# Optimization experiments

Measured on AMD Instinct MI355X. Metric: run time of the kernel, lower is better.

The kernel has to match this reference:

```python
import jax, jax.numpy as jnp
import numpy as np
from jax import lax

# ---- config (mirrors cfg) ----
NUM_LEVELS = 4
DS = 2            # DS_FACTOR
T = 16            # TILE_SIZE
SR = 4            # SEARCH_RADIUS
PADD = 1
SW = 0.1          # SPATIAL_WEIGHT
GR = 2            # GAUSS_RADIUS
SIGMA = 1.0
SS = 2 * (SR + PADD) + 1      # 11: padded search grid
SSC = 2 * SR + 1              # 9: cropped search grid
WIN = T + 2 * (SR + PADD)     # 26: gathered window per tile

# ---- subpixel-refinement quadratic-fit filters (from __init__) ----
F_A11 = jnp.asarray(np.array([[1,-2,1],[2,-4,2],[1,-2,1]], np.float32) / 4.0)
F_A22 = jnp.asarray(np.array([[1,2,1],[-2,-4,-2],[1,2,1]], np.float32) / 4.0)
F_A12 = jnp.asarray(np.array([[1,0,-1],[0,0,0],[-1,0,1]], np.float32) / 4.0)
F_B1  = jnp.asarray(np.array([[-1,0,1],[-2,0,2],[-1,0,1]], np.float32) / 8.0)
F_B2  = jnp.asarray(np.array([[-1,-2,-1],[0,0,0],[1,2,1]], np.float32) / 8.0)
F_C   = jnp.asarray(np.array([[-1,2,-1],[2,12,2],[-1,2,-1]], np.float32) / 16.0)


def _gauss_kernel():
    ws = 2 * GR + 1
    ax = np.arange(ws, dtype=np.float32) - GR
    g = np.exp(-(ax ** 2) / (2.0 * SIGMA ** 2))
    k = np.outer(g, g)
    k = k / k.sum()
    return jnp.asarray(k, jnp.float32)


def _pyramid(x):
    """Gaussian pyramid: depthwise gaussian blur + avg-pool(ds) per level."""
    k = _gauss_kernel()[None, None]  # OIHW, C=1
    pad = (2 * GR + 1 - 1) // 2
    pyr = [x]
    for _ in range(NUM_LEVELS - 1):
        y = lax.conv_general_dilated(x, k, (1, 1), [(pad, pad), (pad, pad)],
                                     dimension_numbers=('NCHW', 'OIHW', 'NCHW'))
        n, c, h, w = y.shape
        x = y.reshape(n, c, h // DS, DS, w // DS, DS).mean(axis=(3, 5))
        pyr.append(x)
    return pyr


def _sdist_map():
    ax = (np.arange(SS, dtype=np.float32) - (SR + PADD)) / float(SS)
    return jnp.asarray(ax[:, None] ** 2 + ax[None, :] ** 2, jnp.float32)


def _step(init_offset, src, dst):
    """One pyramid-level block-matching step + subpixel refine."""
    n, nth, ntw, _ = init_offset.shape
    H, W = src.shape[2], src.shape[3]
    oy = jnp.round(init_offset[..., 0]).astype(jnp.int32)
    ox = jnp.round(init_offset[..., 1]).astype(jnp.int32)
    base_y = (jnp.arange(nth, dtype=jnp.int32) * T)[None, :, None]
    base_x = (jnp.arange(ntw, dtype=jnp.int32) * T)[None, None, :]
    y0 = base_y + oy - (SR + PADD)
    x0 = base_x + ox - (SR + PADD)
    Y = jnp.clip(y0[..., None] + jnp.arange(WIN), 0, H - 1)
    X = jnp.clip(x0[..., None] + jnp.arange(WIN), 0, W - 1)
    nidx = jnp.arange(n)[:, None, None, None, None]
    window = dst[:, 0][nidx, Y[..., :, None], X[..., None, :]]
    # source tiles [n,nth,ntw,T,T]
    src_t = src[:, 0].reshape(n, nth, T, ntw, T).transpose(0, 1, 3, 2, 4)
    # all SSxSS candidate tiles from the window (static slide indices)
    sl = jnp.arange(SS)[:, None] + jnp.arange(T)[None, :]  # [SS,T]
    cand = window[:, :, :, sl[:, None, :, None], sl[None, :, None, :]]  # [n,nth,ntw,SS,SS,T,T]
    adist = jnp.mean((cand - src_t[:, :, :, None, None]) ** 2, axis=(-2, -1))
    dist_full = adist + SW * _sdist_map()  # [n,nth,ntw,SS,SS]
    dist = dist_full[:, :, :, PADD:-PADD, PADD:-PADD].reshape(n, nth, ntw, SSC * SSC)
    min_dist = jnp.min(dist, axis=3)
    pk = jnp.argmin(dist, axis=3)
    py = pk // SSC
    px = pk % SSC
    offset = init_offset + jnp.stack([(py - SR).astype(jnp.float32),
                                      (px - SR).astype(jnp.float32)], axis=3)
    # RegionSelection: 3x3 neighborhood of dist_full around (py+PADD, px+PADD)
    ry = (py + PADD)[..., None] + jnp.arange(-1, 2)
    rx = (px + PADD)[..., None] + jnp.arange(-1, 2)
    tyi = jnp.arange(nth)[None, :, None, None, None]
    txi = jnp.arange(ntw)[None, None, :, None, None]
    yreg = dist_full[nidx, tyi, txi, ry[..., :, None], rx[..., None, :]]  # [n,nth,ntw,3,3]
    s = lambda f: jnp.sum(f * yreg, axis=(-2, -1))
    a11 = jax.nn.relu(s(F_A11))
    a22 = jax.nn.relu(s(F_A22))
    a12 = s(F_A12)
    b1 = s(F_B1)
    b2 = s(F_B2)
    det = a11 * a22 - a12 ** 2
    a12z = jnp.where(det < 0, jnp.zeros_like(a12), a12)
    mu_x = -(a22 * b1 - a12z * b2) / det
    mu_y = -(a11 * b2 - a12z * b1) / det
    mu_len = jnp.sqrt(mu_y ** 2 + mu_x ** 2)
    dx = jnp.where(mu_len < 1.0, mu_x, jnp.zeros_like(mu_x))
    dy = jnp.where(mu_len < 1.0, mu_y, jnp.zeros_like(mu_y))
    offset = offset.at[..., 0].add(dy).at[..., 1].add(dx)
    return offset, min_dist


def _inherit(prev_offset, nth, ntw, H, W):
    typ = jnp.arange(nth) // DS
    txp = jnp.arange(ntw) // DS
    off = DS * prev_offset[:, typ[:, None], txp[None, :], :]
    iy = (jnp.arange(nth, dtype=jnp.float32) * T)[None, :, None]
    ix = (jnp.arange(ntw, dtype=jnp.float32) * T)[None, None, :]
    dy = jnp.clip(off[..., 0] + iy, 0.0, float(H - T)) - iy
    dx = jnp.clip(off[..., 1] + ix, 0.0, float(W - T)) - ix
    return jnp.round(jnp.stack([dy, dx], axis=3))


def _align(src, dst):
    ps = _pyramid(src)
    pd = _pyramid(dst)
    offset = None
    min_dist = None
    for level in range(NUM_LEVELS - 1, -1, -1):
        s, d = ps[level], pd[level]
        n, _, h, w = s.shape
        nth = int(np.ceil(h / T))
        ntw = int(np.ceil(w / T))
        if level == NUM_LEVELS - 1:
            init = jnp.zeros((n, nth, ntw, 2), jnp.float32)
        else:
            init = _inherit(offset, nth, ntw, h, w)
        offset, min_dist = _step(init, s, d)
    # nearest-neighbor upsample by TILE_SIZE to per-pixel maps
    pixel_off = jnp.repeat(jnp.repeat(offset, T, axis=1), T, axis=2)   # [n,H,W,2]
    pixel_dist = jnp.repeat(jnp.repeat(min_dist, T, axis=1), T, axis=2)  # [n,H,W]
    return pixel_off, pixel_dist


def setup_inputs() -> dict:
    key = jax.random.key(0)
    k1, k2 = jax.random.split(key)
    src = jax.random.uniform(k1, (4, 1, 512, 512), jnp.float32)
    dst = jax.random.uniform(k2, (4, 1, 512, 512), jnp.float32)
    return {"src": src, "dst": dst}


def reference(src, dst):
    return _align(src, dst)
```

## Files before the change

### kernel.cpp

```cpp
#include <hip/hip_runtime.h>


#define NB 4
#define NPIX (NB * 512 * 512)

constexpr float H6[6] = {
    0.027244342f, 0.149345013f, 0.323410645f,
    0.323410645f, 0.149345013f, 0.027244342f
};

__global__ void __launch_bounds__(256, 4)
pyramid_kernel(const float* __restrict__ src, const float* __restrict__ dst,
               float* __restrict__ ws) {
    __shared__ float smem[8160];
    float* patch = smem;
    float* tmpH1 = smem + 5520;
    float* l1    = smem;
    float* tmpH2 = smem + 1232;
    float* l2    = smem + 1792;
    float* tmpH3 = smem + 2032;

    float* sL1 = ws;
    float* dL1 = sL1 + 4 * 65536;
    float* sL2 = dL1 + 4 * 65536;
    float* dL2 = sL2 + 4 * 16384;
    float* sL3 = dL2 + 4 * 16384;
    float* dL3 = sL3 + 4 * 4096;

    const int bx = blockIdx.x, by = blockIdx.y, z = blockIdx.z;
    const int t = threadIdx.x;
    const float* in = (z < 4) ? (src + (size_t)z * 262144) : (dst + (size_t)(z - 4) * 262144);
    float* oL1 = ((z < 4) ? sL1 : dL1) + (size_t)(z & 3) * 65536;
    float* oL2 = ((z < 4) ? sL2 : dL2) + (size_t)(z & 3) * 16384;
    float* oL3 = ((z < 4) ? sL3 : dL3) + (size_t)(z & 3) * 4096;

    {
        const int oy = by * 32 - 14, ox = bx * 64 - 14;
        for (int idx = t; idx < 5520; idx += 256) {
            int r = idx / 92, c = idx - r * 92;
            int gy = oy + r, gx = ox + c;
            float v = 0.f;
            if ((unsigned)gy < 512u && (unsigned)gx < 512u) v = in[gy * 512 + gx];
            patch[r * 92 + c] = v;
        }
    }
    __syncthreads();
    for (int idx = t; idx < 2640; idx += 256) {
        int r = idx / 44, v = idx - r * 44;
        const float* p = &patch[r * 92 + 2 * v];
        float a = 0.f;
        #pragma unroll
        for (int bq = 0; bq < 6; ++bq) a = fmaf(H6[bq], p[bq], a);
        tmpH1[r * 44 + v] = a;
    }
    __syncthreads();
    {
        const int oy = by * 16 - 6, ox = bx * 32 - 6;
        for (int idx = t; idx < 1232; idx += 256) {
            int u = idx / 44, v = idx - u * 44;
            float a = 0.f;
            int y1 = oy + u, x1 = ox + v;
            if ((unsigned)y1 < 256u && (unsigned)x1 < 256u) {
                #pragma unroll
                for (int bq = 0; bq < 6; ++bq) a = fmaf(H6[bq], tmpH1[(2 * u + bq) * 44 + v], a);
            }
            l1[u * 44 + v] = a;
        }
    }
    __syncthreads();
    {
        #pragma unroll
        for (int k = 0; k < 2; ++k) {
            int idx = t + k * 256;
            int u = idx >> 5, v = idx & 31;
            oL1[(by * 16 + u) * 256 + bx * 32 + v] = l1[(6 + u) * 44 + 6 + v];
        }
    }
    for (int idx = t; idx < 560; idx += 256) {
        int r = idx / 20, v = idx - r * 20;
        const float* p = &l1[r * 44 + 2 * v];
        float a = 0.f;
        #pragma unroll
        for (int bq = 0; bq < 6; ++bq) a = fmaf(H6[bq], p[bq], a);
        tmpH2[r * 20 + v] = a;
    }
    __syncthreads();
    {
        const int oy = by * 8 - 2, ox = bx * 16 - 2;
        if (t < 240) {
            int u = t / 20, v = t - u * 20;
            float a = 0.f;
            int y2 = oy + u, x2 = ox + v;
            if ((unsigned)y2 < 128u && (unsigned)x2 < 128u) {
                #pragma unroll
                for (int bq = 0; bq < 6; ++bq) a = fmaf(H6[bq], tmpH2[(2 * u + bq) * 20 + v], a);
            }
            l2[u * 20 + v] = a;
        }
    }
    __syncthreads();
    if (t < 128) {
        int u = t >> 4, v = t & 15;
        oL2[(by * 8 + u) * 128 + bx * 16 + v] = l2[(2 + u) * 20 + 2 + v];
    } else if (t < 224) {
        int idx = t - 128;
        int r = idx >> 3, v = idx & 7;
        const float* p = &l2[r * 20 + 2 * v];
        float a = 0.f;
        #pragma unroll
        for (int bq = 0; bq < 6; ++bq) a = fmaf(H6[bq], p[bq], a);
        tmpH3[r * 8 + v] = a;
    }
    __syncthreads();
    if (t < 32) {
        int u = t >> 3, v = t & 7;
        float a = 0.f;
        #pragma unroll
        for (int bq = 0; bq < 6; ++bq) a = fmaf(H6[bq], tmpH3[(2 * u + bq) * 8 + v], a);
        oL3[(by * 4 + u) * 64 + bx * 8 + v] = a;
    }
}

__device__ __forceinline__ void inherit_off(int ty, int tx, int H,
                                            float pary, float parx,
                                            float& dyf, float& dxf) {
    float iy = (float)(ty * 16), ix = (float)(tx * 16);
    dyf = rintf(fminf(fmaxf(2.f * pary + iy, 0.f), (float)(H - 16)) - iy);
    dxf = rintf(fminf(fmaxf(2.f * parx + ix, 0.f), (float)(H - 16)) - ix);
}

template<int NL>
__device__ __forceinline__ void load_win(const float* __restrict__ dimg, int H,
                                         int y0, int x0, float* win, int lt) {
    const int c = lt & 31;
    const int r0 = lt >> 5;
    constexpr int RSTEP = NL / 32;
    if (c < 26) {
        const int gx = min(max(x0 + c, 0), H - 1);
        #pragma unroll
        for (int k = 0; k < (26 + RSTEP - 1) / RSTEP; ++k) {
            const int rr = r0 + k * RSTEP;
            if (rr < 26) {
                const int gy = min(max(y0 + rr, 0), H - 1);
                win[rr * 28 + c] = dimg[gy * H + gx];
            }
        }
    }
}

template<bool FULL>
__device__ __forceinline__ void ssd_dist(const float* win, const float* st,
                                         float* dist, int lt) {
    const int dy = FULL ? (lt >> 4) : (lt >> 3);
    if (dy < 11) {
        float acc[11];
        #pragma unroll
        for (int q = 0; q < 11; ++q) acc[q] = 0.f;
        constexpr int ROWS = FULL ? 1 : 2;
        #pragma unroll
        for (int rr = 0; rr < ROWS; ++rr) {
            const int i = FULL ? (lt & 15) : ((lt & 7) * 2 + rr);
            float w[28], s[16];
            const float4* wp = (const float4*)&win[(dy + i) * 28];
            #pragma unroll
            for (int q = 0; q < 7; ++q) ((float4*)w)[q] = wp[q];
            const float4* sp = (const float4*)&st[i * 20];
            #pragma unroll
            for (int q = 0; q < 4; ++q) ((float4*)s)[q] = sp[q];
            #pragma unroll
            for (int dx = 0; dx < 11; ++dx) {
                #pragma unroll
                for (int j = 0; j < 16; ++j) {
                    float d = w[dx + j] - s[j];
                    acc[dx] = fmaf(d, d, acc[dx]);
                }
            }
        }
        constexpr int MMAX = FULL ? 8 : 4;
        #pragma unroll
        for (int m = 1; m <= MMAX; m <<= 1) {
            #pragma unroll
            for (int dx = 0; dx < 11; ++dx) acc[dx] += __shfl_xor(acc[dx], m);
        }
        const bool leader = FULL ? ((lt & 15) == 0) : ((lt & 7) == 0);
        if (leader) {
            float ay = (float)(dy - 5) * (1.f / 11.f);
            #pragma unroll
            for (int dx = 0; dx < 11; ++dx) {
                float ax = (float)(dx - 5) * (1.f / 11.f);
                dist[dy * 11 + dx] = acc[dx] * (1.f / 256.f) + 0.1f * (ay * ay + ax * ax);
            }
        }
    }
}

__device__ __forceinline__ void argmin_refine(const float* dist, int lt,
                                              float dyf, float dxf,
                                              float& roy, float& rox, float& rod) {
    const int l = lt & 63;
    float bv; int bk;
    {
        int k = l;
        int py = k / 9, px = k - (k / 9) * 9;
        bv = dist[(py + 1) * 11 + (px + 1)]; bk = k;
        k = l + 64;
        if (k < 81) {
            py = k / 9; px = k - (k / 9) * 9;
            float d = dist[(py + 1) * 11 + (px + 1)];
            if (d < bv) { bv = d; bk = k; }
        }
    }
    #pragma unroll
    for (int m = 1; m <= 32; m <<= 1) {
        float ov = __shfl_xor(bv, m);
        int   ok = __shfl_xor(bk, m);
        if (ov < bv || (ov == bv && ok < bk)) { bv = ov; bk = ok; }
    }
    {
        int py = bk / 9, px = bk - (bk / 9) * 9;
        float y00 = dist[(py + 0) * 11 + (px + 0)], y01 = dist[(py + 0) * 11 + (px + 1)], y02 = dist[(py + 0) * 11 + (px + 2)];
        float y10 = dist[(py + 1) * 11 + (px + 0)], y11 = dist[(py + 1) * 11 + (px + 1)], y12 = dist[(py + 1) * 11 + (px + 2)];
        float y20 = dist[(py + 2) * 11 + (px + 0)], y21 = dist[(py + 2) * 11 + (px + 1)], y22 = dist[(py + 2) * 11 + (px + 2)];

        float a11 = (y00 - 2.f * y01 + y02 + 2.f * y10 - 4.f * y11 + 2.f * y12 + y20 - 2.f * y21 + y22) * 0.25f;
        a11 = fmaxf(a11, 0.f);
        float a22 = (y00 + 2.f * y01 + y02 - 2.f * y10 - 4.f * y11 - 2.f * y12 + y20 + 2.f * y21 + y22) * 0.25f;
        a22 = fmaxf(a22, 0.f);
        float a12 = (y00 - y02 - y20 + y22) * 0.25f;
        float b1  = (-y00 + y02 - 2.f * y10 + 2.f * y12 - y20 + y22) * 0.125f;
        float b2  = (-y00 - 2.f * y01 - y02 + y20 + 2.f * y21 + y22) * 0.125f;

        float det  = a11 * a22 - a12 * a12;
        float a12z = (det < 0.f) ? 0.f : a12;
        float mu_x = -(a22 * b1 - a12z * b2) / det;
        float mu_y = -(a11 * b2 - a12z * b1) / det;
        float mu_len = sqrtf(mu_x * mu_x + mu_y * mu_y);
        float addx = (mu_len < 1.f) ? mu_x : 0.f;
        float addy = (mu_len < 1.f) ? mu_y : 0.f;

        roy = dyf + (float)(py - 4) + addy;
        rox = dxf + (float)(px - 4) + addx;
        rod = bv;
    }
}

__global__ void __launch_bounds__(256, 4)
step_chain_kernel(const float* __restrict__ src, const float* __restrict__ dst,
                  const float* __restrict__ ws, float* __restrict__ out) {
    __shared__ float smem[6520];

    const float* sL1 = ws;
    const float* dL1 = sL1 + 4 * 65536;
    const float* sL2 = dL1 + 4 * 65536;
    const float* dL2 = sL2 + 4 * 16384;
    const float* sL3 = dL2 + 4 * 16384;
    const float* dL3 = sL3 + 4 * 4096;

    const int gid = blockIdx.x;
    const int b   = gid >> 8;
    const int ty1 = (gid >> 4) & 15;
    const int tx1 = gid & 15;
    const int t    = threadIdx.x;
    const int slot = t >> 7;
    const int s_t  = t & 127;

    float* win_c  = smem;
    float* winA   = smem + 728 + (2 * slot + 0) * 728;
    float* winB   = smem + 728 + (2 * slot + 1) * 728;
    float* dist_c = smem + 3640;
    float* distA  = smem + 3768 + (2 * slot + 0) * 128;
    float* distB  = smem + 3768 + (2 * slot + 1) * 128;
    float* stL3 = smem + 4280;
    float* stL2 = smem + 4600;
    float* stL1 = smem + 4920;
    float* st0  = smem + 5240;

    const float* s0 = src + (size_t)b * 262144; const float* d0 = dst + (size_t)b * 262144;
    const float* s1 = sL1 + (size_t)b * 65536;  const float* d1 = dL1 + (size_t)b * 65536;
    const float* s2 = sL2 + (size_t)b * 16384;  const float* d2 = dL2 + (size_t)b * 16384;
    const float* s3 = sL3 + (size_t)b * 4096;   const float* d3 = dL3 + (size_t)b * 4096;

    {
        const int it = t & 63, r = it >> 2, q = t & 3;
        const int c = t >> 6;
        const int ty0 = 2 * ty1 + (c >> 1), tx0 = 2 * tx1 + (c & 1);
        const float4* p0 = (const float4*)(s0 + (size_t)(ty0 * 16 + r) * 512 + tx0 * 16);
        ((float4*)&st0[c * 320 + r * 20])[q] = p0[q];
        if (t < 64) {
            const float4* p = (const float4*)(s3 + (size_t)((ty1 >> 2) * 16 + r) * 64 + (tx1 >> 2) * 16);
            ((float4*)&stL3[r * 20])[q] = p[q];
        } else if (t < 128) {
            const float4* p = (const float4*)(s2 + (size_t)((ty1 >> 1) * 16 + r) * 128 + (tx1 >> 1) * 16);
            ((float4*)&stL2[r * 20])[q] = p[q];
        } else if (t < 192) {
            const float4* p = (const float4*)(s1 + (size_t)(ty1 * 16 + r) * 256 + tx1 * 16);
            ((float4*)&stL1[r * 20])[q] = p[q];
        }
    }

    float oy, ox, od;
    {
        load_win<256>(d3, 64, (ty1 >> 2) * 16 - 5, (tx1 >> 2) * 16 - 5, win_c, t);
        __syncthreads();
        ssd_dist<true>(win_c, stL3, dist_c, t);
        __syncthreads();
        argmin_refine(dist_c, t, 0.f, 0.f, oy, ox, od);
    }
    {
        float dyf, dxf; inherit_off(ty1 >> 1, tx1 >> 1, 128, oy, ox, dyf, dxf);
        load_win<256>(d2, 128, (ty1 >> 1) * 16 + (int)dyf - 5, (tx1 >> 1) * 16 + (int)dxf - 5, win_c, t);
        __syncthreads();
        ssd_dist<true>(win_c, stL2, dist_c, t);
        __syncthreads();
        argmin_refine(dist_c, t, dyf, dxf, oy, ox, od);
    }
    {
        float dyf, dxf; inherit_off(ty1, tx1, 256, oy, ox, dyf, dxf);
        load_win<256>(d1, 256, ty1 * 16 + (int)dyf - 5, tx1 * 16 + (int)dxf - 5, win_c, t);
        __syncthreads();
        ssd_dist<true>(win_c, stL1, dist_c, t);
        __syncthreads();
        argmin_refine(dist_c, t, dyf, dxf, oy, ox, od);
    }

    const int tyA = 2 * ty1,     txA = 2 * tx1 + slot;
    const int tyB = 2 * ty1 + 1, txB = 2 * tx1 + slot;
    float dyfA, dxfA, dyfB, dxfB;
    inherit_off(tyA, txA, 512, oy, ox, dyfA, dxfA);
    inherit_off(tyB, txB, 512, oy, ox, dyfB, dxfB);
    load_win<128>(d0, 512, tyA * 16 + (int)dyfA - 5, txA * 16 + (int)dxfA - 5, winA, s_t);
    load_win<128>(d0, 512, tyB * 16 + (int)dyfB - 5, txB * 16 + (int)dxfB - 5, winB, s_t);
    __syncthreads();
    ssd_dist<false>(winA, st0 + (0 * 2 + slot) * 320, distA, s_t);
    __syncthreads();
    ssd_dist<false>(winB, st0 + (1 * 2 + slot) * 320, distB, s_t);
    __syncthreads();

    const int r = s_t >> 3, c2 = (s_t & 7) * 2;
    {
        float oyA, oxA, odA;
        argmin_refine(distA, s_t, dyfA, dxfA, oyA, oxA, odA);
        int pyy = tyA * 16 + r, pxx = txA * 16 + c2;
        size_t pi = ((size_t)(b * 512 + pyy)) * 512 + pxx;
        float2 o; o.x = oyA; o.y = oxA;
        ((float2*)out)[pi]     = o;
        ((float2*)out)[pi + 1] = o;
        float2 dd; dd.x = odA; dd.y = odA;
        *(float2*)(out + (size_t)NPIX * 2 + pi) = dd;
    }
    {
        float oyB, oxB, odB;
        argmin_refine(distB, s_t, dyfB, dxfB, oyB, oxB, odB);
        int pyy = tyB * 16 + r, pxx = txB * 16 + c2;
        size_t pi = ((size_t)(b * 512 + pyy)) * 512 + pxx;
        float2 o; o.x = oyB; o.y = oxB;
        ((float2*)out)[pi]     = o;
        ((float2*)out)[pi + 1] = o;
        float2 dd; dd.x = odB; dd.y = odB;
        *(float2*)(out + (size_t)NPIX * 2 + pi) = dd;
    }
}

extern "C" void kernel_launch(void* const* d_in, const int* in_sizes, int n_in,
                              void* d_out, int out_size, void* d_ws, size_t ws_size,
                              hipStream_t stream) {
    const float* src = (const float*)d_in[0];
    const float* dst = (const float*)d_in[1];
    float* out = (float*)d_out;
    float* ws  = (float*)d_ws;

    hipLaunchKernelGGL(pyramid_kernel, dim3(8, 16, 8), dim3(256), 0, stream, src, dst, ws);
    hipLaunchKernelGGL(step_chain_kernel, dim3(1024), dim3(256), 0, stream, src, dst, ws, out);
}
```

Measured before the change: 104.5 us.

## Split coarse pyramid levels into a separate seed kernel to avoid redundant work

The coarse levels 3 and 2 of the block-matching chain used to be recomputed by every step_chain block, even though four blocks share the same level-2 tile and sixteen share the same level-3 tile. A new seed_kernel computes them once per level-2 tile and writes the offsets to workspace. step_chain_kernel then reads the seed offset and runs only levels 1 and 0. This removes duplicated coarse-level work and some shared memory, at the cost of an extra kernel launch and a global round trip.

```diff
diff --git a/kernel.cpp b/kernel.cpp
--- a/kernel.cpp
+++ b/kernel.cpp
@@ -3,6 +3,7 @@
 
 #define NB 4
 #define NPIX (NB * 512 * 512)
+#define OFFS_BASE 1212416
 
 constexpr float H6[6] = {
     0.027244342f, 0.149345013f, 0.323410645f,
@@ -245,16 +246,67 @@
 }
 
 __global__ void __launch_bounds__(256, 4)
-step_chain_kernel(const float* __restrict__ src, const float* __restrict__ dst,
-                  const float* __restrict__ ws, float* __restrict__ out) {
-    __shared__ float smem[6520];
-
-    const float* sL1 = ws;
-    const float* dL1 = sL1 + 4 * 65536;
-    const float* sL2 = dL1 + 4 * 65536;
+seed_kernel(const float* __restrict__ ws_ro, float* __restrict__ ws) {
+    __shared__ float smem[1496];
+    float* win_c  = smem;
+    float* dist_c = smem + 728;
+    float* stL3   = smem + 856;
+    float* stL2   = smem + 1176;
+
+    const float* sL2 = ws_ro + 4 * 65536 + 4 * 65536;
     const float* dL2 = sL2 + 4 * 16384;
     const float* sL3 = dL2 + 4 * 16384;
     const float* dL3 = sL3 + 4 * 4096;
+    float* offs = ws + OFFS_BASE;
+
+    const int gid = blockIdx.x;
+    const int b   = gid >> 6;
+    const int ty2 = (gid >> 3) & 7;
+    const int tx2 = gid & 7;
+    const int t   = threadIdx.x;
+
+    const float* s2 = sL2 + (size_t)b * 16384;  const float* d2 = dL2 + (size_t)b * 16384;
+    const float* s3 = sL3 + (size_t)b * 4096;   const float* d3 = dL3 + (size_t)b * 4096;
+
+    {
+        const int it = t & 63, r = it >> 2, q = t & 3;
+        if (t < 64) {
+            const float4* p = (const float4*)(s3 + (size_t)((ty2 >> 1) * 16 + r) * 64 + (tx2 >> 1) * 16);
+            ((float4*)&stL3[r * 20])[q] = p[q];
+        } else if (t < 128) {
+            const float4* p = (const float4*)(s2 + (size_t)(ty2 * 16 + r) * 128 + tx2 * 16);
+            ((float4*)&stL2[r * 20])[q] = p[q];
+        }
+    }
+
+    float oy, ox, od;
+    load_win<256>(d3, 64, (ty2 >> 1) * 16 - 5, (tx2 >> 1) * 16 - 5, win_c, t);
+    __syncthreads();
+    ssd_dist<true>(win_c, stL3, dist_c, t);
+    __syncthreads();
+    argmin_refine(dist_c, t, 0.f, 0.f, oy, ox, od);
+    {
+        float dyf, dxf; inherit_off(ty2, tx2, 128, oy, ox, dyf, dxf);
+        load_win<256>(d2, 128, ty2 * 16 + (int)dyf - 5, tx2 * 16 + (int)dxf - 5, win_c, t);
+        __syncthreads();
+        ssd_dist<true>(win_c, stL2, dist_c, t);
+        __syncthreads();
+        argmin_refine(dist_c, t, dyf, dxf, oy, ox, od);
+    }
+    if (t == 0) {
+        const int oi = ((b * 8 + ty2) * 8 + tx2) * 2;
+        offs[oi]     = oy;
+        offs[oi + 1] = ox;
+    }
+}
+
+__global__ void __launch_bounds__(256, 4)
+step_chain_kernel(const float* __restrict__ src, const float* __restrict__ dst,
+                  const float* __restrict__ ws, float* __restrict__ out) {
+    __shared__ float smem[5880];
+
+    const float* sL1 = ws;
+    const float* offs = ws + OFFS_BASE;
 
     const int gid = blockIdx.x;
     const int b   = gid >> 8;
@@ -270,15 +322,15 @@
     float* dist_c = smem + 3640;
     float* distA  = smem + 3768 + (2 * slot + 0) * 128;
     float* distB  = smem + 3768 + (2 * slot + 1) * 128;
-    float* stL3 = smem + 4280;
-    float* stL2 = smem + 4600;
-    float* stL1 = smem + 4920;
-    float* st0  = smem + 5240;
+    float* stL1 = smem + 4280;
+    float* st0  = smem + 4600;
 
     const float* s0 = src + (size_t)b * 262144; const float* d0 = dst + (size_t)b * 262144;
-    const float* s1 = sL1 + (size_t)b * 65536;  const float* d1 = dL1 + (size_t)b * 65536;
-    const float* s2 = sL2 + (size_t)b * 16384;  const float* d2 = dL2 + (size_t)b * 16384;
-    const float* s3 = sL3 + (size_t)b * 4096;   const float* d3 = dL3 + (size_t)b * 4096;
+    const float* s1 = sL1 + (size_t)b * 65536;
+    const float* d1 = sL1 + 4 * 65536 + (size_t)b * 65536;
+
+    const int oi = ((b * 8 + (ty1 >> 1)) * 8 + (tx1 >> 1)) * 2;
+    const float poy = offs[oi], pox = offs[oi + 1];
 
     {
         const int it = t & 63, r = it >> 2, q = t & 3;
@@ -287,12 +339,6 @@
         const float4* p0 = (const float4*)(s0 + (size_t)(ty0 * 16 + r) * 512 + tx0 * 16);
         ((float4*)&st0[c * 320 + r * 20])[q] = p0[q];
         if (t < 64) {
-            const float4* p = (const float4*)(s3 + (size_t)((ty1 >> 2) * 16 + r) * 64 + (tx1 >> 2) * 16);
-            ((float4*)&stL3[r * 20])[q] = p[q];
-        } else if (t < 128) {
-            const float4* p = (const float4*)(s2 + (size_t)((ty1 >> 1) * 16 + r) * 128 + (tx1 >> 1) * 16);
-            ((float4*)&stL2[r * 20])[q] = p[q];
-        } else if (t < 192) {
             const float4* p = (const float4*)(s1 + (size_t)(ty1 * 16 + r) * 256 + tx1 * 16);
             ((float4*)&stL1[r * 20])[q] = p[q];
         }
@@ -300,22 +346,7 @@
 
     float oy, ox, od;
     {
-        load_win<256>(d3, 64, (ty1 >> 2) * 16 - 5, (tx1 >> 2) * 16 - 5, win_c, t);
-        __syncthreads();
-        ssd_dist<true>(win_c, stL3, dist_c, t);
-        __syncthreads();
-        argmin_refine(dist_c, t, 0.f, 0.f, oy, ox, od);
-    }
-    {
-        float dyf, dxf; inherit_off(ty1 >> 1, tx1 >> 1, 128, oy, ox, dyf, dxf);
-        load_win<256>(d2, 128, (ty1 >> 1) * 16 + (int)dyf - 5, (tx1 >> 1) * 16 + (int)dxf - 5, win_c, t);
-        __syncthreads();
-        ssd_dist<true>(win_c, stL2, dist_c, t);
-        __syncthreads();
-        argmin_refine(dist_c, t, dyf, dxf, oy, ox, od);
-    }
-    {
-        float dyf, dxf; inherit_off(ty1, tx1, 256, oy, ox, dyf, dxf);
+        float dyf, dxf; inherit_off(ty1, tx1, 256, poy, pox, dyf, dxf);
         load_win<256>(d1, 256, ty1 * 16 + (int)dyf - 5, tx1 * 16 + (int)dxf - 5, win_c, t);
         __syncthreads();
         ssd_dist<true>(win_c, stL1, dist_c, t);
@@ -370,5 +401,6 @@
     float* ws  = (float*)d_ws;
 
     hipLaunchKernelGGL(pyramid_kernel, dim3(8, 16, 8), dim3(256), 0, stream, src, dst, ws);
+    hipLaunchKernelGGL(seed_kernel, dim3(256), dim3(256), 0, stream, (const float*)ws, ws);
     hipLaunchKernelGGL(step_chain_kernel, dim3(1024), dim3(256), 0, stream, src, dst, ws, out);
 }
```

After: 102.5 us (median of 2 runs). No clear change (-1.9%).
